# Optimization experiments

Measured on AMD Instinct MI355X. Metric: run time of the kernel, lower is better.

The kernel has to match this reference:

```python
import jax, jax.numpy as jnp
import numpy as np

N_H_NODES = 100000
N_G_NODES = 100000
N_EDGES = 1000000
N_GRAPHS = 64
N_H, N_G, N_X, N_U = 64, 64, 8, 16
IN_DIM = N_H + N_G + N_X + N_U  # 152
N_X_OUT = 1


def setup_inputs() -> dict:
    key = jax.random.key(0)
    ks = jax.random.split(key, 10)
    return {
        "x_h": jax.random.normal(ks[0], (N_H_NODES, N_H), dtype=jnp.float32),
        "x_g": jax.random.normal(ks[1], (N_G_NODES, N_G), dtype=jnp.float32),
        "edge_attr": jax.random.normal(ks[2], (N_EDGES, N_X), dtype=jnp.float32),
        "u": jax.random.normal(ks[3], (N_GRAPHS, N_U), dtype=jnp.float32),
        "edge_index": jax.random.randint(ks[4], (2, N_EDGES), 0, N_H_NODES, dtype=jnp.int64),
        "batch_e": jax.random.randint(ks[5], (N_EDGES,), 0, N_GRAPHS, dtype=jnp.int64),
        "W1": jax.random.normal(ks[6], (IN_DIM, N_X_OUT), dtype=jnp.float32) * 0.08,
        "b1": jnp.zeros((N_X_OUT,), dtype=jnp.float32),
        "W2": jax.random.normal(ks[7], (N_X_OUT, N_X_OUT), dtype=jnp.float32) * 0.5,
        "b2": jnp.zeros((N_X_OUT,), dtype=jnp.float32),
    }


def reference(x_h, x_g, edge_attr, u, edge_index, batch_e, W1, b1, W2, b2):
    src = edge_index[0]
    tgt = edge_index[1]
    # gather node/global features per edge and concat: [E, n_h+n_g+n_x+n_u]
    feat = jnp.concatenate([x_h[src], x_g[tgt], edge_attr, u[batch_e]], axis=1)
    h = feat @ W1 + b1                       # [E, 1]
    h = jnp.where(h >= 0, h, 0.1 * h)        # LeakyReLU(0.1)
    out = h @ W2 + b2                        # [E, 1]
    return out
```

## Files before the change

### kernel.cpp

```cpp
#include <hip/hip_runtime.h>
#include <hip/hip_bf16.h>


#define TPB 256
#define NB_EDGE 1024
#define NB_NODE 1024

typedef float f32x2 __attribute__((ext_vector_type(2)));
typedef float f32x4 __attribute__((ext_vector_type(4)));

__device__ __forceinline__ float dot4(float4 a, float4 b) {
    return a.x * b.x + a.y * b.y + a.z * b.z + a.w * b.w;
}

__global__ void __launch_bounds__(TPB, 8)
k1_partials(const float* __restrict__ xh, const float* __restrict__ xg,
            const float* __restrict__ edge_attr, const float* __restrict__ u,
            const int* __restrict__ batch_e,
            const float* __restrict__ W1, const float* __restrict__ b1,
            float* __restrict__ ph, float* __restrict__ pg,
            float* __restrict__ se,
            int nh, int ng, int ngr, int E) {
    if ((int)blockIdx.x < NB_EDGE) {
        __shared__ float pu_s[256];
        if ((int)threadIdx.x < ngr) {
            const float4* uv = reinterpret_cast<const float4*>(u + (size_t)threadIdx.x * 16);
            const float4* wu = reinterpret_cast<const float4*>(W1 + 136);
            float s = dot4(uv[0], wu[0]) + dot4(uv[1], wu[1])
                    + dot4(uv[2], wu[2]) + dot4(uv[3], wu[3]);
            pu_s[threadIdx.x] = s + b1[0];
        }
        __syncthreads();

        const float* wx = W1 + 128;
        const float w0 = wx[0], w1 = wx[1], w2 = wx[2], w3 = wx[3];
        const float w4 = wx[4], w5 = wx[5], w6 = wx[6], w7 = wx[7];

        const int tid    = blockIdx.x * TPB + threadIdx.x;
        const int stride = NB_EDGE * TPB * 2;
        for (int base = tid * 2; base < E; base += stride) {
            if (base + 1 < E) {
                const f32x4* eap = reinterpret_cast<const f32x4*>(edge_attr + (size_t)base * 8);
                f32x4 a0 = eap[0], a1 = eap[1], a2 = eap[2], a3 = eap[3];
                int2 gv = *reinterpret_cast<const int2*>(batch_e + base);
                float s0 = pu_s[gv.x]
                         + a0.x * w0 + a0.y * w1 + a0.z * w2 + a0.w * w3
                         + a1.x * w4 + a1.y * w5 + a1.z * w6 + a1.w * w7;
                float s1 = pu_s[gv.y]
                         + a2.x * w0 + a2.y * w1 + a2.z * w2 + a2.w * w3
                         + a3.x * w4 + a3.y * w5 + a3.z * w6 + a3.w * w7;
                f32x2 sv; sv.x = s0; sv.y = s1;
                *reinterpret_cast<f32x2*>(se + base) = sv;
            } else {
                const float* a = edge_attr + (size_t)base * 8;
                int g = batch_e[base];
                se[base] = pu_s[g]
                         + a[0] * w0 + a[1] * w1 + a[2] * w2 + a[3] * w3
                         + a[4] * w4 + a[5] * w5 + a[6] * w6 + a[7] * w7;
            }
        }
    } else {
        const int bid     = blockIdx.x - NB_EDGE;
        const int gid     = bid * TPB + threadIdx.x;
        const int group   = gid >> 4;
        const int q       = gid & 15;
        const int ngroups = (NB_NODE * TPB) >> 4;
        const int total   = nh + ng;
        for (int r = group; r < total; r += ngroups) {
            const float* srcp = (r < nh) ? xh + (size_t)r * 64
                                         : xg + (size_t)(r - nh) * 64;
            const float* wp   = (r < nh) ? W1 : W1 + 64;
            float4 v  = reinterpret_cast<const float4*>(srcp)[q];
            float4 wv = reinterpret_cast<const float4*>(wp)[q];
            float s = dot4(v, wv);
            s += __shfl_xor(s, 1);
            s += __shfl_xor(s, 2);
            s += __shfl_xor(s, 4);
            s += __shfl_xor(s, 8);
            if (q == 0) {
                if (r < nh) ph[r] = s;
                else        pg[r - nh] = s;
            }
        }
    }
}

__global__ void __launch_bounds__(TPB, 8)
k2_finalize(const int* __restrict__ edge_index,
            const float* __restrict__ se,
            const float* __restrict__ W2, const float* __restrict__ b2,
            const float* __restrict__ ph, const float* __restrict__ pg,
            float* __restrict__ out, int E) {
    const int t = blockIdx.x * TPB + threadIdx.x;
    const int base = t * 4;
    if (base >= E) return;

    const float w2s = W2[0], b2s = b2[0];

    if (base + 3 < E) {
        int4 sv = *reinterpret_cast<const int4*>(edge_index + base);
        int4 tv = *reinterpret_cast<const int4*>(edge_index + E + base);
        f32x4 sev = *reinterpret_cast<const f32x4*>(se + base);

        float pp[4] = {ph[sv.x], ph[sv.y], ph[sv.z], ph[sv.w]};
        float qq[4] = {pg[tv.x], pg[tv.y], pg[tv.z], pg[tv.w]};
        float s4[4] = {sev.x, sev.y, sev.z, sev.w};

        f32x4 hv;
        float res[4];
#pragma unroll
        for (int i = 0; i < 4; ++i) {
            float h = s4[i] + pp[i] + qq[i];
            h = (h >= 0.0f) ? h : 0.1f * h;
            res[i] = h * w2s + b2s;
        }
        hv.x = res[0]; hv.y = res[1]; hv.z = res[2]; hv.w = res[3];
        *reinterpret_cast<f32x4*>(out + base) = hv;
    } else {
        for (int e = base; e < E; ++e) {
            float h = se[e] + ph[edge_index[e]] + pg[edge_index[E + e]];
            h = (h >= 0.0f) ? h : 0.1f * h;
            out[e] = h * w2s + b2s;
        }
    }
}

__global__ void edge_fallback(const int* __restrict__ edge_index,
                              const int* __restrict__ batch_e,
                              const float* __restrict__ xh,
                              const float* __restrict__ xg,
                              const float* __restrict__ edge_attr,
                              const float* __restrict__ u,
                              const float* __restrict__ W1,
                              const float* __restrict__ b1,
                              const float* __restrict__ W2,
                              const float* __restrict__ b2,
                              float* __restrict__ out,
                              int E) {
    int e = blockIdx.x * blockDim.x + threadIdx.x;
    if (e >= E) return;
    int s = edge_index[e];
    int t = edge_index[E + e];
    int g = batch_e[e];
    float h = b1[0];
    const float* hs = xh + (size_t)s * 64;
    const float* gt = xg + (size_t)t * 64;
#pragma unroll 8
    for (int j = 0; j < 64; ++j) h += hs[j] * W1[j];
#pragma unroll 8
    for (int j = 0; j < 64; ++j) h += gt[j] * W1[64 + j];
    const float* ea = edge_attr + (size_t)e * 8;
#pragma unroll
    for (int j = 0; j < 8; ++j) h += ea[j] * W1[128 + j];
    const float* ug = u + (size_t)g * 16;
#pragma unroll
    for (int j = 0; j < 16; ++j) h += ug[j] * W1[136 + j];
    h = (h >= 0.0f) ? h : 0.1f * h;
    out[e] = h * W2[0] + b2[0];
}

extern "C" void kernel_launch(void* const* d_in, const int* in_sizes, int n_in,
                              void* d_out, int out_size, void* d_ws, size_t ws_size,
                              hipStream_t stream) {
    const float* x_h       = (const float*)d_in[0];
    const float* x_g       = (const float*)d_in[1];
    const float* edge_attr = (const float*)d_in[2];
    const float* u         = (const float*)d_in[3];
    const int*   edge_idx  = (const int*)d_in[4];
    const int*   batch_e   = (const int*)d_in[5];
    const float* W1        = (const float*)d_in[6];
    const float* b1        = (const float*)d_in[7];
    const float* W2        = (const float*)d_in[8];
    const float* b2        = (const float*)d_in[9];
    float* out = (float*)d_out;

    const int E   = in_sizes[5];
    const int nh  = in_sizes[0] / 64;
    const int ng  = in_sizes[1] / 64;
    const int ngr = in_sizes[3] / 16;

    size_t need = ((size_t)nh + ng + E) * sizeof(float);
    if (ws_size >= need && ngr <= 256) {
        float* ph = (float*)d_ws;
        float* pg = ph + nh;
        float* se = pg + ng;

        k1_partials<<<NB_EDGE + NB_NODE, TPB, 0, stream>>>(
            x_h, x_g, edge_attr, u, batch_e, W1, b1, ph, pg, se,
            nh, ng, ngr, E);

        int threads = (E + 3) / 4;
        int eb = (threads + TPB - 1) / TPB;
        k2_finalize<<<eb, TPB, 0, stream>>>(edge_idx, se, W2, b2, ph, pg, out, E);
    } else {
        int eb = (E + TPB - 1) / TPB;
        edge_fallback<<<eb, TPB, 0, stream>>>(edge_idx, batch_e, x_h, x_g, edge_attr, u,
                                              W1, b1, W2, b2, out, E);
    }
}
```

Baseline: 30.85 us.

## Move edge-attr and global partials into edge kernel, drop se intermediate

```diff
diff --git a/kernel.cpp b/kernel.cpp
--- a/kernel.cpp
+++ b/kernel.cpp
@@ -3,10 +3,7 @@
 
 
 #define TPB 256
-#define NB_EDGE 1024
-#define NB_NODE 1024
 
-typedef float f32x2 __attribute__((ext_vector_type(2)));
 typedef float f32x4 __attribute__((ext_vector_type(4)));
 
 __device__ __forceinline__ float dot4(float4 a, float4 b) {
@@ -14,103 +11,86 @@
 }
 
 __global__ void __launch_bounds__(TPB, 8)
-k1_partials(const float* __restrict__ xh, const float* __restrict__ xg,
-            const float* __restrict__ edge_attr, const float* __restrict__ u,
-            const int* __restrict__ batch_e,
-            const float* __restrict__ W1, const float* __restrict__ b1,
-            float* __restrict__ ph, float* __restrict__ pg,
-            float* __restrict__ se,
-            int nh, int ng, int ngr, int E) {
-    if ((int)blockIdx.x < NB_EDGE) {
-        __shared__ float pu_s[256];
-        if ((int)threadIdx.x < ngr) {
-            const float4* uv = reinterpret_cast<const float4*>(u + (size_t)threadIdx.x * 16);
-            const float4* wu = reinterpret_cast<const float4*>(W1 + 136);
-            float s = dot4(uv[0], wu[0]) + dot4(uv[1], wu[1])
-                    + dot4(uv[2], wu[2]) + dot4(uv[3], wu[3]);
-            pu_s[threadIdx.x] = s + b1[0];
-        }
-        __syncthreads();
+k_nodes(const float* __restrict__ xh, const float* __restrict__ xg,
+        const float* __restrict__ W1,
+        float* __restrict__ ph, float* __restrict__ pg,
+        int nh, int ng) {
+    const int gid     = blockIdx.x * TPB + threadIdx.x;
+    const int group   = gid >> 4;
+    const int q       = gid & 15;
+    const int ngroups = (gridDim.x * TPB) >> 4;
 
-        const float* wx = W1 + 128;
-        const float w0 = wx[0], w1 = wx[1], w2 = wx[2], w3 = wx[3];
-        const float w4 = wx[4], w5 = wx[5], w6 = wx[6], w7 = wx[7];
+    const float4 wh = reinterpret_cast<const float4*>(W1)[q];
+    const float4 wg = reinterpret_cast<const float4*>(W1 + 64)[q];
 
-        const int tid    = blockIdx.x * TPB + threadIdx.x;
-        const int stride = NB_EDGE * TPB * 2;
-        for (int base = tid * 2; base < E; base += stride) {
-            if (base + 1 < E) {
-                const f32x4* eap = reinterpret_cast<const f32x4*>(edge_attr + (size_t)base * 8);
-                f32x4 a0 = eap[0], a1 = eap[1], a2 = eap[2], a3 = eap[3];
-                int2 gv = *reinterpret_cast<const int2*>(batch_e + base);
-                float s0 = pu_s[gv.x]
-                         + a0.x * w0 + a0.y * w1 + a0.z * w2 + a0.w * w3
-                         + a1.x * w4 + a1.y * w5 + a1.z * w6 + a1.w * w7;
-                float s1 = pu_s[gv.y]
-                         + a2.x * w0 + a2.y * w1 + a2.z * w2 + a2.w * w3
-                         + a3.x * w4 + a3.y * w5 + a3.z * w6 + a3.w * w7;
-                f32x2 sv; sv.x = s0; sv.y = s1;
-                *reinterpret_cast<f32x2*>(se + base) = sv;
-            } else {
-                const float* a = edge_attr + (size_t)base * 8;
-                int g = batch_e[base];
-                se[base] = pu_s[g]
-                         + a[0] * w0 + a[1] * w1 + a[2] * w2 + a[3] * w3
-                         + a[4] * w4 + a[5] * w5 + a[6] * w6 + a[7] * w7;
-            }
-        }
-    } else {
-        const int bid     = blockIdx.x - NB_EDGE;
-        const int gid     = bid * TPB + threadIdx.x;
-        const int group   = gid >> 4;
-        const int q       = gid & 15;
-        const int ngroups = (NB_NODE * TPB) >> 4;
-        const int total   = nh + ng;
-        for (int r = group; r < total; r += ngroups) {
-            const float* srcp = (r < nh) ? xh + (size_t)r * 64
-                                         : xg + (size_t)(r - nh) * 64;
-            const float* wp   = (r < nh) ? W1 : W1 + 64;
-            float4 v  = reinterpret_cast<const float4*>(srcp)[q];
-            float4 wv = reinterpret_cast<const float4*>(wp)[q];
-            float s = dot4(v, wv);
-            s += __shfl_xor(s, 1);
-            s += __shfl_xor(s, 2);
-            s += __shfl_xor(s, 4);
-            s += __shfl_xor(s, 8);
-            if (q == 0) {
-                if (r < nh) ph[r] = s;
-                else        pg[r - nh] = s;
-            }
-        }
+    for (int r = group; r < nh; r += ngroups) {
+        float4 v = reinterpret_cast<const float4*>(xh + (size_t)r * 64)[q];
+        float s = dot4(v, wh);
+        s += __shfl_xor(s, 1);
+        s += __shfl_xor(s, 2);
+        s += __shfl_xor(s, 4);
+        s += __shfl_xor(s, 8);
+        if (q == 0) ph[r] = s;
+    }
+    for (int r = group; r < ng; r += ngroups) {
+        float4 v = reinterpret_cast<const float4*>(xg + (size_t)r * 64)[q];
+        float s = dot4(v, wg);
+        s += __shfl_xor(s, 1);
+        s += __shfl_xor(s, 2);
+        s += __shfl_xor(s, 4);
+        s += __shfl_xor(s, 8);
+        if (q == 0) pg[r - 0] = s;
     }
 }
 
 __global__ void __launch_bounds__(TPB, 8)
-k2_finalize(const int* __restrict__ edge_index,
-            const float* __restrict__ se,
-            const float* __restrict__ W2, const float* __restrict__ b2,
-            const float* __restrict__ ph, const float* __restrict__ pg,
-            float* __restrict__ out, int E) {
+k_edges(const int* __restrict__ edge_index, const int* __restrict__ batch_e,
+        const float* __restrict__ edge_attr, const float* __restrict__ u,
+        const float* __restrict__ W1, const float* __restrict__ b1,
+        const float* __restrict__ W2, const float* __restrict__ b2,
+        const float* __restrict__ ph, const float* __restrict__ pg,
+        float* __restrict__ out, int ngr, int E) {
+    __shared__ float pu_s[256];
+    if ((int)threadIdx.x < ngr) {
+        const float4* uv = reinterpret_cast<const float4*>(u + (size_t)threadIdx.x * 16);
+        const float4* wu = reinterpret_cast<const float4*>(W1 + 136);
+        float s = dot4(uv[0], wu[0]) + dot4(uv[1], wu[1])
+                + dot4(uv[2], wu[2]) + dot4(uv[3], wu[3]);
+        pu_s[threadIdx.x] = s + b1[0];
+    }
+    __syncthreads();
+
     const int t = blockIdx.x * TPB + threadIdx.x;
     const int base = t * 4;
     if (base >= E) return;
 
+    const float* wx = W1 + 128;
+    const float w0 = wx[0], w1 = wx[1], w2 = wx[2], w3 = wx[3];
+    const float w4 = wx[4], w5 = wx[5], w6 = wx[6], w7 = wx[7];
     const float w2s = W2[0], b2s = b2[0];
 
     if (base + 3 < E) {
         int4 sv = *reinterpret_cast<const int4*>(edge_index + base);
         int4 tv = *reinterpret_cast<const int4*>(edge_index + E + base);
-        f32x4 sev = *reinterpret_cast<const f32x4*>(se + base);
+        int4 gv = *reinterpret_cast<const int4*>(batch_e + base);
 
         float pp[4] = {ph[sv.x], ph[sv.y], ph[sv.z], ph[sv.w]};
         float qq[4] = {pg[tv.x], pg[tv.y], pg[tv.z], pg[tv.w]};
-        float s4[4] = {sev.x, sev.y, sev.z, sev.w};
+        float rr[4] = {pu_s[gv.x], pu_s[gv.y], pu_s[gv.z], pu_s[gv.w]};
+
+        const f32x4* eap = reinterpret_cast<const f32x4*>(edge_attr + (size_t)base * 8);
+        f32x4 ea[8];
+#pragma unroll
+        for (int j = 0; j < 8; ++j) ea[j] = eap[j];
 
         f32x4 hv;
         float res[4];
 #pragma unroll
         for (int i = 0; i < 4; ++i) {
-            float h = s4[i] + pp[i] + qq[i];
+            f32x4 a0 = ea[2 * i], a1 = ea[2 * i + 1];
+            float h = pp[i] + qq[i] + rr[i]
+                    + a0.x * w0 + a0.y * w1 + a0.z * w2 + a0.w * w3
+                    + a1.x * w4 + a1.y * w5 + a1.z * w6 + a1.w * w7;
             h = (h >= 0.0f) ? h : 0.1f * h;
             res[i] = h * w2s + b2s;
         }
@@ -118,7 +98,13 @@
         *reinterpret_cast<f32x4*>(out + base) = hv;
     } else {
         for (int e = base; e < E; ++e) {
-            float h = se[e] + ph[edge_index[e]] + pg[edge_index[E + e]];
+            int s  = edge_index[e];
+            int tg = edge_index[E + e];
+            int g  = batch_e[e];
+            const float* a = edge_attr + (size_t)e * 8;
+            float h = ph[s] + pg[tg] + pu_s[g]
+                    + a[0] * w0 + a[1] * w1 + a[2] * w2 + a[3] * w3
+                    + a[4] * w4 + a[5] * w5 + a[6] * w6 + a[7] * w7;
             h = (h >= 0.0f) ? h : 0.1f * h;
             out[e] = h * w2s + b2s;
         }
@@ -179,19 +165,20 @@
     const int ng  = in_sizes[1] / 64;
     const int ngr = in_sizes[3] / 16;
 
-    size_t need = ((size_t)nh + ng + E) * sizeof(float);
+    size_t need = ((size_t)nh + ng) * sizeof(float);
     if (ws_size >= need && ngr <= 256) {
         float* ph = (float*)d_ws;
         float* pg = ph + nh;
-        float* se = pg + ng;
 
-        k1_partials<<<NB_EDGE + NB_NODE, TPB, 0, stream>>>(
-            x_h, x_g, edge_attr, u, batch_e, W1, b1, ph, pg, se,
-            nh, ng, ngr, E);
+        int maxn = (nh > ng) ? nh : ng;
+        int nb = (maxn * 16 + TPB - 1) / TPB;
+        if (nb > 2048) nb = 2048;
+        k_nodes<<<nb, TPB, 0, stream>>>(x_h, x_g, W1, ph, pg, nh, ng);
 
         int threads = (E + 3) / 4;
         int eb = (threads + TPB - 1) / TPB;
-        k2_finalize<<<eb, TPB, 0, stream>>>(edge_idx, se, W2, b2, ph, pg, out, E);
+        k_edges<<<eb, TPB, 0, stream>>>(edge_idx, batch_e, edge_attr, u,
+                                        W1, b1, W2, b2, ph, pg, out, ngr, E);
     } else {
         int eb = (E + TPB - 1) / TPB;
         edge_fallback<<<eb, TPB, 0, stream>>>(edge_idx, batch_e, x_h, x_g, edge_attr, u,
```

Measured after the change: 30.04 us. 1.03x faster.
